# Optimization experiments

Hardware: AMD Instinct MI355X
Metric: run time of the kernel (lower is better)

The kernel has to match this reference:

```python
import jax, jax.numpy as jnp
import numpy as np

WS = (8, 8)          # window size
NHEAD = 6
D_MODEL = 192

def _rel_pos_index(ws):
    coords = np.stack(np.meshgrid(np.arange(ws[0]), np.arange(ws[1]), indexing='ij'))  # (2, wh, ww)
    cf = coords.reshape(2, -1)                          # (2, N)
    rel = cf[:, :, None] - cf[:, None, :]               # (2, N, N)
    rel = rel.transpose(1, 2, 0).astype(np.int64)       # (N, N, 2)
    rel[:, :, 0] += ws[0] - 1
    rel[:, :, 1] += ws[1] - 1
    rel[:, :, 0] *= 2 * ws[1] - 1
    return rel.sum(-1)                                  # (N, N)

REL_IDX = jnp.asarray(_rel_pos_index(WS))

def setup_inputs() -> dict:
    key = jax.random.key(0)
    ks = jax.random.split(key, 6)
    B, H, W, C = 4, 256, 256, D_MODEL
    x = jax.random.normal(ks[0], (B, H * W, C), dtype=jnp.float32)
    qkv_w = jax.random.normal(ks[1], (3 * C, C), dtype=jnp.float32) * 0.02
    qkv_b = jnp.zeros((3 * C,), dtype=jnp.float32)
    proj_w = jax.random.normal(ks[2], (C, C), dtype=jnp.float32) * 0.02
    proj_b = jnp.zeros((C,), dtype=jnp.float32)
    n_bias = (2 * WS[0] - 1) * (2 * WS[1] - 1)
    rpb_table = jax.random.normal(ks[3], (n_bias, NHEAD), dtype=jnp.float32) * 0.02
    return {"x": x, "qkv_w": qkv_w, "qkv_b": qkv_b, "proj_w": proj_w,
            "proj_b": proj_b, "rpb_table": rpb_table, "H": H, "W": W}

def reference(x, qkv_w, qkv_b, proj_w, proj_b, rpb_table, H, W):
    B, Ni, C = x.shape
    h, d = NHEAD, C // NHEAD
    wh, ww = WS
    nH, nW = H // wh, W // ww
    N = wh * ww
    # window partition: (B, H, W, C) -> (B*nH*nW, N, C)
    xw = x.reshape(B, nH, wh, nW, ww, C).transpose(0, 1, 3, 2, 4, 5).reshape(-1, N, C)
    qkv = xw @ qkv_w.T + qkv_b                           # (B_, N, 3C)
    B_ = xw.shape[0]
    qkv = qkv.reshape(B_, N, 3, h, d).transpose(2, 0, 3, 1, 4)  # (3, B_, h, N, d)
    q, k, v = qkv[0], qkv[1], qkv[2]
    scale = d ** -0.5
    attn = jnp.einsum('bhnd,bhmd->bhnm', q, k) * scale   # (B_, h, N, N)
    bias = rpb_table[REL_IDX.reshape(-1)].reshape(N, N, h).transpose(2, 0, 1)  # (h, N, N)
    attn = jax.nn.softmax(attn + bias[None], axis=-1)
    out = jnp.einsum('bhnm,bhmd->bhnd', attn, v)         # (B_, h, N, d)
    out = out.transpose(0, 2, 1, 3).reshape(B_, N, C)
    out = out @ proj_w.T + proj_b
    # window reverse: (B*nH*nW, N, C) -> (B, H*W, C)
    out = out.reshape(B, nH, nW, wh, ww, C).transpose(0, 1, 3, 2, 4, 5).reshape(B, Ni, C)
    return out
```

## Files before the change

### kernel.cpp

```cpp
#include <hip/hip_runtime.h>

#define CDIM 192
#define NHEAD 6

typedef __bf16 bf16x8 __attribute__((ext_vector_type(8)));
typedef float f32x4 __attribute__((ext_vector_type(4)));

#define HB     78848
#define Q_OFF  0
#define K_OFF  25600
#define VT_OFF 51200
#define SMEM_BYTES (2 * HB)
#define XS  200
#define QS  200
#define KS  200
#define VTS 72
#define AOS 200
#define PS  72
#define OFS 196
#define SCALE 0.17677669529663687f

__device__ __forceinline__ unsigned short f2b(float f) {
    unsigned int u = __float_as_uint(f);
    u = (u + 0x7FFFu + ((u >> 16) & 1u)) >> 16;
    return (unsigned short)u;
}

#define WS_W1   0
#define WS_W2   221184
#define WS_BIAS 294912

__global__ void prep(const float* __restrict__ qkv_w, const float* __restrict__ proj_w,
                     const float* __restrict__ rpb,
                     unsigned short* __restrict__ W1, unsigned short* __restrict__ W2,
                     float* __restrict__ BIAS) {
    int t = blockIdx.x * 256 + threadIdx.x;
    if (t < 110592) { W1[t] = f2b(qkv_w[t]); return; }
    t -= 110592;
    if (t < 36864)  { W2[t] = f2b(proj_w[t]); return; }
    t -= 36864;
    {
        int h = t >> 12, ij = t & 4095;
        int i = ij >> 6, j = ij & 63;
        int idx = ((i >> 3) - (j >> 3) + 7) * 15 + ((i & 7) - (j & 7) + 7);
        BIAS[t] = rpb[idx * NHEAD + h];
    }
}

__global__ __launch_bounds__(512)
void win_attn(const float* __restrict__ x,
              const unsigned short* __restrict__ qkv_w,
              const float* __restrict__ qkv_b,
              const unsigned short* __restrict__ proj_w,
              const float* __restrict__ proj_b,
              const float* __restrict__ bias,
              float* __restrict__ out)
{
    extern __shared__ __align__(16) char smem[];

    const int tid  = threadIdx.x;
    const int wv   = tid >> 6;
    const int lane = tid & 63;
    const int l15  = lane & 15;
    const int g    = lane >> 4;
    const int g4   = g << 2;
    const int g8   = g << 3;

    long long base[2];
    #pragma unroll
    for (int w = 0; w < 2; ++w) {
        int wid = blockIdx.x * 2 + w;
        int b   = wid >> 10;
        int wy  = (wid >> 5) & 31;
        int wx  = wid & 31;
        base[w] = (long long)(b * 65536 + wy * 8 * 256 + wx * 8) * CDIM;
    }

    #pragma unroll
    for (int w = 0; w < 2; ++w) {
        __bf16* xk = (__bf16*)(smem + w * HB + K_OFF);
        #pragma unroll
        for (int r = 0; r < 6; ++r) {
            int i = tid + r * 512;
            int t = i / 48, part = i - t * 48;
            int iy = t >> 3, ix = t & 7;
            f32x4 v = *(const f32x4*)(x + base[w] + (iy * 256 + ix) * CDIM + part * 4);
            __bf16* dst = xk + t * XS + part * 4;
            dst[0] = (__bf16)v[0]; dst[1] = (__bf16)v[1];
            dst[2] = (__bf16)v[2]; dst[3] = (__bf16)v[3];
        }
    }
    __syncthreads();

    {
        const int qstart_lut[8] = {0, 5, 10, 15, 20, 25, 30, 31};
        const int start = qstart_lut[wv];

        f32x4 acc[2][4][5];
        #pragma unroll
        for (int w = 0; w < 2; ++w)
            #pragma unroll
            for (int mt = 0; mt < 4; ++mt)
                #pragma unroll
                for (int jn = 0; jn < 5; ++jn)
                    acc[w][mt][jn] = (f32x4){0.f, 0.f, 0.f, 0.f};

        #pragma unroll
        for (int kk = 0; kk < 6; ++kk) {
            bf16x8 bw[5];
            #pragma unroll
            for (int jn = 0; jn < 5; ++jn) {
                int o = (start + jn) * 16 + l15;
                bw[jn] = *(const bf16x8*)((const __bf16*)qkv_w + o * CDIM + kk * 32 + g8);
            }
            #pragma unroll
            for (int w = 0; w < 2; ++w) {
                const __bf16* xk = (const __bf16*)(smem + w * HB + K_OFF);
                bf16x8 aa[4];
                #pragma unroll
                for (int mt = 0; mt < 4; ++mt)
                    aa[mt] = *(const bf16x8*)(xk + (mt * 16 + l15) * XS + kk * 32 + g8);
                #pragma unroll
                for (int jn = 0; jn < 5; ++jn)
                    #pragma unroll
                    for (int mt = 0; mt < 4; ++mt)
                        acc[w][mt][jn] = __builtin_amdgcn_mfma_f32_16x16x32_bf16(aa[mt], bw[jn], acc[w][mt][jn], 0, 0, 0);
            }
        }
        __syncthreads();

        #pragma unroll
        for (int jn = 0; jn < 5; ++jn) {
            int nt = start + jn;
            int o  = nt * 16 + l15;
            float qb = qkv_b[o];
            #pragma unroll
            for (int w = 0; w < 2; ++w) {
                __bf16* ql  = (__bf16*)(smem + w * HB + Q_OFF);
                __bf16* kl  = (__bf16*)(smem + w * HB + K_OFF);
                __bf16* vtw = (__bf16*)(smem + w * HB + VT_OFF);
                #pragma unroll
                for (int mt = 0; mt < 4; ++mt) {
                    #pragma unroll
                    for (int rr = 0; rr < 4; ++rr) {
                        int tr = mt * 16 + g4 + rr;
                        float val = acc[w][mt][jn][rr] + qb;
                        if (nt < 12)       ql[tr * QS + o] = (__bf16)val;
                        else if (nt < 24)  kl[tr * KS + (o - 192)] = (__bf16)val;
                        else               vtw[(o - 384) * VTS + tr] = (__bf16)val;
                    }
                }
            }
        }
    }
    __syncthreads();

    f32x4 sh[2][3][4];
    #pragma unroll
    for (int w = 0; w < 2; ++w) {
        const __bf16* ql = (const __bf16*)(smem + w * HB + Q_OFF);
        const __bf16* kl = (const __bf16*)(smem + w * HB + K_OFF);
        #pragma unroll
        for (int u = 0; u < 3; ++u) {
            int gu = wv * 3 + u;
            int hu = gu >> 2;
            int rb = gu & 3;

            bf16x8 aq = *(const bf16x8*)(ql + (rb * 16 + l15) * QS + hu * 32 + g8);
            #pragma unroll
            for (int ni = 0; ni < 4; ++ni) {
                bf16x8 bk = *(const bf16x8*)(kl + (ni * 16 + l15) * KS + hu * 32 + g8);
                sh[w][u][ni] = __builtin_amdgcn_mfma_f32_16x16x32_bf16(aq, bk, (f32x4){0.f, 0.f, 0.f, 0.f}, 0, 0, 0);
            }

            const float* brow = bias + hu * 4096;
            #pragma unroll
            for (int rr = 0; rr < 4; ++rr) {
                int row = rb * 16 + g4 + rr;
                float v0 = sh[w][u][0][rr] * SCALE + brow[row * 64 +  0 + l15];
                float v1 = sh[w][u][1][rr] * SCALE + brow[row * 64 + 16 + l15];
                float v2 = sh[w][u][2][rr] * SCALE + brow[row * 64 + 32 + l15];
                float v3 = sh[w][u][3][rr] * SCALE + brow[row * 64 + 48 + l15];
                float m = fmaxf(fmaxf(v0, v1), fmaxf(v2, v3));
                m = fmaxf(m, __shfl_xor(m, 1));
                m = fmaxf(m, __shfl_xor(m, 2));
                m = fmaxf(m, __shfl_xor(m, 4));
                m = fmaxf(m, __shfl_xor(m, 8));
                v0 = __expf(v0 - m); v1 = __expf(v1 - m);
                v2 = __expf(v2 - m); v3 = __expf(v3 - m);
                float s = v0 + v1 + v2 + v3;
                s += __shfl_xor(s, 1); s += __shfl_xor(s, 2);
                s += __shfl_xor(s, 4); s += __shfl_xor(s, 8);
                float inv = 1.0f / s;
                sh[w][u][0][rr] = v0 * inv;
                sh[w][u][1][rr] = v1 * inv;
                sh[w][u][2][rr] = v2 * inv;
                sh[w][u][3][rr] = v3 * inv;
            }
        }
    }
    __syncthreads();

    #pragma unroll
    for (int w = 0; w < 2; ++w) {
        __bf16* ph  = (__bf16*)(smem + w * HB + Q_OFF) + wv * (16 * PS);
        const __bf16* vtw = (const __bf16*)(smem + w * HB + VT_OFF);
        __bf16* aob = (__bf16*)(smem + w * HB + K_OFF);
        #pragma unroll
        for (int u = 0; u < 3; ++u) {
            int gu = wv * 3 + u;
            int hu = gu >> 2;
            int rb = gu & 3;

            #pragma unroll
            for (int rr = 0; rr < 4; ++rr) {
                int pr = (g4 + rr) * PS;
                ph[pr +  0 + l15] = (__bf16)sh[w][u][0][rr];
                ph[pr + 16 + l15] = (__bf16)sh[w][u][1][rr];
                ph[pr + 32 + l15] = (__bf16)sh[w][u][2][rr];
                ph[pr + 48 + l15] = (__bf16)sh[w][u][3][rr];
            }
            __threadfence_block();

            f32x4 oacc[2];
            oacc[0] = (f32x4){0.f, 0.f, 0.f, 0.f};
            oacc[1] = (f32x4){0.f, 0.f, 0.f, 0.f};
            #pragma unroll
            for (int kk = 0; kk < 2; ++kk) {
                bf16x8 pa = *(const bf16x8*)(ph + l15 * PS + kk * 32 + g8);
                #pragma unroll
                for (int nj = 0; nj < 2; ++nj) {
                    bf16x8 bv = *(const bf16x8*)(vtw + (hu * 32 + nj * 16 + l15) * VTS + kk * 32 + g8);
                    oacc[nj] = __builtin_amdgcn_mfma_f32_16x16x32_bf16(pa, bv, oacc[nj], 0, 0, 0);
                }
            }
            __threadfence_block();
            #pragma unroll
            for (int nj = 0; nj < 2; ++nj)
                #pragma unroll
                for (int rr = 0; rr < 4; ++rr)
                    aob[(rb * 16 + g4 + rr) * AOS + hu * 32 + nj * 16 + l15] = (__bf16)oacc[nj][rr];
        }
    }
    __syncthreads();

    {
        const int pstart_lut[8] = {0, 2, 4, 6, 8, 10, 10, 10};
        const int start = pstart_lut[wv];

        f32x4 pacc[2][4][2];
        #pragma unroll
        for (int w = 0; w < 2; ++w)
            #pragma unroll
            for (int mt = 0; mt < 4; ++mt)
                #pragma unroll
                for (int jn = 0; jn < 2; ++jn)
                    pacc[w][mt][jn] = (f32x4){0.f, 0.f, 0.f, 0.f};

        #pragma unroll
        for (int kk = 0; kk < 6; ++kk) {
            bf16x8 bw[2];
            #pragma unroll
            for (int jn = 0; jn < 2; ++jn) {
                int o = (start + jn) * 16 + l15;
                bw[jn] = *(const bf16x8*)((const __bf16*)proj_w + o * CDIM + kk * 32 + g8);
            }
            #pragma unroll
            for (int w = 0; w < 2; ++w) {
                const __bf16* aob = (const __bf16*)(smem + w * HB + K_OFF);
                bf16x8 aa[4];
                #pragma unroll
                for (int mt = 0; mt < 4; ++mt)
                    aa[mt] = *(const bf16x8*)(aob + (mt * 16 + l15) * AOS + kk * 32 + g8);
                #pragma unroll
                for (int jn = 0; jn < 2; ++jn)
                    #pragma unroll
                    for (int mt = 0; mt < 4; ++mt)
                        pacc[w][mt][jn] = __builtin_amdgcn_mfma_f32_16x16x32_bf16(aa[mt], bw[jn], pacc[w][mt][jn], 0, 0, 0);
            }
        }
        __syncthreads();

        #pragma unroll
        for (int jn = 0; jn < 2; ++jn) {
            int o = (start + jn) * 16 + l15;
            float pb = proj_b[o];
            #pragma unroll
            for (int w = 0; w < 2; ++w) {
                float* stagef = (float*)(smem + w * HB);
                #pragma unroll
                for (int mt = 0; mt < 4; ++mt)
                    #pragma unroll
                    for (int rr = 0; rr < 4; ++rr) {
                        int tr = mt * 16 + g4 + rr;
                        stagef[tr * OFS + o] = pacc[w][mt][jn][rr] + pb;
                    }
            }
        }
    }
    __syncthreads();

    #pragma unroll
    for (int w = 0; w < 2; ++w) {
        const float* stagef = (const float*)(smem + w * HB);
        #pragma unroll
        for (int r = 0; r < 6; ++r) {
            int i = tid + r * 512;
            int t = i / 48, part = i - t * 48;
            int iy = t >> 3, ix = t & 7;
            *(f32x4*)(out + base[w] + (iy * 256 + ix) * CDIM + part * 4) =
                *(const f32x4*)(stagef + t * OFS + part * 4);
        }
    }
}

extern "C" void kernel_launch(void* const* d_in, const int* in_sizes, int n_in,
                              void* d_out, int out_size, void* d_ws, size_t ws_size,
                              hipStream_t stream) {
    const float* x      = (const float*)d_in[0];
    const float* qkv_w  = (const float*)d_in[1];
    const float* qkv_b  = (const float*)d_in[2];
    const float* proj_w = (const float*)d_in[3];
    const float* proj_b = (const float*)d_in[4];
    const float* rpb    = (const float*)d_in[5];
    float* outp = (float*)d_out;

    char* ws = (char*)d_ws;
    unsigned short* W1 = (unsigned short*)(ws + WS_W1);
    unsigned short* W2 = (unsigned short*)(ws + WS_W2);
    float* BIAS = (float*)(ws + WS_BIAS);

    hipFuncSetAttribute((const void*)win_attn,
                        hipFuncAttributeMaxDynamicSharedMemorySize, SMEM_BYTES);

    prep<<<672, 256, 0, stream>>>(qkv_w, proj_w, rpb, W1, W2, BIAS);
    win_attn<<<2048, 512, SMEM_BYTES, stream>>>(x, W1, qkv_b, W2, proj_b, BIAS, outp);
}
```

Before: 371.7 us.

## Load x directly into MFMA operands and process windows sequentially to cut registers

The fp32 input tile is no longer staged through shared memory as bf16. Each wave now reads its x rows straight from global memory, converts them to bf16 in registers and feeds them to the QKV MFMAs, which removes the staging pass and one block barrier. The QKV and attention phases now run one window at a time, so the accumulator and score arrays are half as large, aiming to lower register pressure. The cost is that every wave re-reads the whole x tile from global memory or cache, and the weight fragments are loaded once per window instead of being shared across both.

```diff
diff --git a/kernel.cpp b/kernel.cpp
--- a/kernel.cpp
+++ b/kernel.cpp
@@ -11,7 +11,6 @@
 #define K_OFF  25600
 #define VT_OFF 51200
 #define SMEM_BYTES (2 * HB)
-#define XS  200
 #define QS  200
 #define KS  200
 #define VTS 72
@@ -24,6 +23,13 @@
     unsigned int u = __float_as_uint(f);
     u = (u + 0x7FFFu + ((u >> 16) & 1u)) >> 16;
     return (unsigned short)u;
+}
+
+__device__ __forceinline__ bf16x8 cvt8(f32x4 a, f32x4 b) {
+    bf16x8 r;
+    r[0] = (__bf16)a[0]; r[1] = (__bf16)a[1]; r[2] = (__bf16)a[2]; r[3] = (__bf16)a[3];
+    r[4] = (__bf16)b[0]; r[5] = (__bf16)b[1]; r[6] = (__bf16)b[2]; r[7] = (__bf16)b[3];
+    return r;
 }
 
 #define WS_W1   0
@@ -76,75 +82,58 @@
         base[w] = (long long)(b * 65536 + wy * 8 * 256 + wx * 8) * CDIM;
     }
 
-    #pragma unroll
-    for (int w = 0; w < 2; ++w) {
-        __bf16* xk = (__bf16*)(smem + w * HB + K_OFF);
-        #pragma unroll
-        for (int r = 0; r < 6; ++r) {
-            int i = tid + r * 512;
-            int t = i / 48, part = i - t * 48;
-            int iy = t >> 3, ix = t & 7;
-            f32x4 v = *(const f32x4*)(x + base[w] + (iy * 256 + ix) * CDIM + part * 4);
-            __bf16* dst = xk + t * XS + part * 4;
-            dst[0] = (__bf16)v[0]; dst[1] = (__bf16)v[1];
-            dst[2] = (__bf16)v[2]; dst[3] = (__bf16)v[3];
-        }
-    }
-    __syncthreads();
-
     {
         const int qstart_lut[8] = {0, 5, 10, 15, 20, 25, 30, 31};
         const int start = qstart_lut[wv];
 
-        f32x4 acc[2][4][5];
-        #pragma unroll
-        for (int w = 0; w < 2; ++w)
+        #pragma unroll
+        for (int w = 0; w < 2; ++w) {
+            const float* xr[4];
+            #pragma unroll
+            for (int mt = 0; mt < 4; ++mt) {
+                int t0 = mt * 16 + l15;
+                xr[mt] = x + base[w] + ((t0 >> 3) * 256 + (t0 & 7)) * CDIM;
+            }
+
+            f32x4 acc[4][5];
             #pragma unroll
             for (int mt = 0; mt < 4; ++mt)
                 #pragma unroll
                 for (int jn = 0; jn < 5; ++jn)
-                    acc[w][mt][jn] = (f32x4){0.f, 0.f, 0.f, 0.f};
-
-        #pragma unroll
-        for (int kk = 0; kk < 6; ++kk) {
-            bf16x8 bw[5];
-            #pragma unroll
-            for (int jn = 0; jn < 5; ++jn) {
-                int o = (start + jn) * 16 + l15;
-                bw[jn] = *(const bf16x8*)((const __bf16*)qkv_w + o * CDIM + kk * 32 + g8);
-            }
-            #pragma unroll
-            for (int w = 0; w < 2; ++w) {
-                const __bf16* xk = (const __bf16*)(smem + w * HB + K_OFF);
+                    acc[mt][jn] = (f32x4){0.f, 0.f, 0.f, 0.f};
+
+            #pragma unroll
+            for (int kk = 0; kk < 6; ++kk) {
                 bf16x8 aa[4];
                 #pragma unroll
-                for (int mt = 0; mt < 4; ++mt)
-                    aa[mt] = *(const bf16x8*)(xk + (mt * 16 + l15) * XS + kk * 32 + g8);
-                #pragma unroll
-                for (int jn = 0; jn < 5; ++jn)
+                for (int mt = 0; mt < 4; ++mt) {
+                    f32x4 lo = *(const f32x4*)(xr[mt] + kk * 32 + g8);
+                    f32x4 hi = *(const f32x4*)(xr[mt] + kk * 32 + g8 + 4);
+                    aa[mt] = cvt8(lo, hi);
+                }
+                #pragma unroll
+                for (int jn = 0; jn < 5; ++jn) {
+                    int o = (start + jn) * 16 + l15;
+                    bf16x8 bw = *(const bf16x8*)((const __bf16*)qkv_w + o * CDIM + kk * 32 + g8);
                     #pragma unroll
                     for (int mt = 0; mt < 4; ++mt)
-                        acc[w][mt][jn] = __builtin_amdgcn_mfma_f32_16x16x32_bf16(aa[mt], bw[jn], acc[w][mt][jn], 0, 0, 0);
-            }
-        }
-        __syncthreads();
-
-        #pragma unroll
-        for (int jn = 0; jn < 5; ++jn) {
-            int nt = start + jn;
-            int o  = nt * 16 + l15;
-            float qb = qkv_b[o];
-            #pragma unroll
-            for (int w = 0; w < 2; ++w) {
-                __bf16* ql  = (__bf16*)(smem + w * HB + Q_OFF);
-                __bf16* kl  = (__bf16*)(smem + w * HB + K_OFF);
-                __bf16* vtw = (__bf16*)(smem + w * HB + VT_OFF);
+                        acc[mt][jn] = __builtin_amdgcn_mfma_f32_16x16x32_bf16(aa[mt], bw, acc[mt][jn], 0, 0, 0);
+                }
+            }
+            __bf16* ql  = (__bf16*)(smem + w * HB + Q_OFF);
+            __bf16* kl  = (__bf16*)(smem + w * HB + K_OFF);
+            __bf16* vtw = (__bf16*)(smem + w * HB + VT_OFF);
+            #pragma unroll
+            for (int jn = 0; jn < 5; ++jn) {
+                int nt = start + jn;
+                int o  = nt * 16 + l15;
+                float qb = qkv_b[o];
                 #pragma unroll
                 for (int mt = 0; mt < 4; ++mt) {
                     #pragma unroll
                     for (int rr = 0; rr < 4; ++rr) {
                         int tr = mt * 16 + g4 + rr;
-                        float val = acc[w][mt][jn][rr] + qb;
+                        float val = acc[mt][jn][rr] + qb;
                         if (nt < 12)       ql[tr * QS + o] = (__bf16)val;
                         else if (nt < 24)  kl[tr * KS + (o - 192)] = (__bf16)val;
                         else               vtw[(o - 384) * VTS + tr] = (__bf16)val;
@@ -155,93 +144,94 @@
     }
     __syncthreads();
 
-    f32x4 sh[2][3][4];
-    #pragma unroll
-    for (int w = 0; w < 2; ++w) {
-        const __bf16* ql = (const __bf16*)(smem + w * HB + Q_OFF);
-        const __bf16* kl = (const __bf16*)(smem + w * HB + K_OFF);
-        #pragma unroll
-        for (int u = 0; u < 3; ++u) {
-            int gu = wv * 3 + u;
-            int hu = gu >> 2;
-            int rb = gu & 3;
-
-            bf16x8 aq = *(const bf16x8*)(ql + (rb * 16 + l15) * QS + hu * 32 + g8);
-            #pragma unroll
-            for (int ni = 0; ni < 4; ++ni) {
-                bf16x8 bk = *(const bf16x8*)(kl + (ni * 16 + l15) * KS + hu * 32 + g8);
-                sh[w][u][ni] = __builtin_amdgcn_mfma_f32_16x16x32_bf16(aq, bk, (f32x4){0.f, 0.f, 0.f, 0.f}, 0, 0, 0);
-            }
-
-            const float* brow = bias + hu * 4096;
-            #pragma unroll
-            for (int rr = 0; rr < 4; ++rr) {
-                int row = rb * 16 + g4 + rr;
-                float v0 = sh[w][u][0][rr] * SCALE + brow[row * 64 +  0 + l15];
-                float v1 = sh[w][u][1][rr] * SCALE + brow[row * 64 + 16 + l15];
-                float v2 = sh[w][u][2][rr] * SCALE + brow[row * 64 + 32 + l15];
-                float v3 = sh[w][u][3][rr] * SCALE + brow[row * 64 + 48 + l15];
-                float m = fmaxf(fmaxf(v0, v1), fmaxf(v2, v3));
-                m = fmaxf(m, __shfl_xor(m, 1));
-                m = fmaxf(m, __shfl_xor(m, 2));
-                m = fmaxf(m, __shfl_xor(m, 4));
-                m = fmaxf(m, __shfl_xor(m, 8));
-                v0 = __expf(v0 - m); v1 = __expf(v1 - m);
-                v2 = __expf(v2 - m); v3 = __expf(v3 - m);
-                float s = v0 + v1 + v2 + v3;
-                s += __shfl_xor(s, 1); s += __shfl_xor(s, 2);
-                s += __shfl_xor(s, 4); s += __shfl_xor(s, 8);
-                float inv = 1.0f / s;
-                sh[w][u][0][rr] = v0 * inv;
-                sh[w][u][1][rr] = v1 * inv;
-                sh[w][u][2][rr] = v2 * inv;
-                sh[w][u][3][rr] = v3 * inv;
-            }
-        }
-    }
-    __syncthreads();
-
-    #pragma unroll
-    for (int w = 0; w < 2; ++w) {
-        __bf16* ph  = (__bf16*)(smem + w * HB + Q_OFF) + wv * (16 * PS);
-        const __bf16* vtw = (const __bf16*)(smem + w * HB + VT_OFF);
-        __bf16* aob = (__bf16*)(smem + w * HB + K_OFF);
-        #pragma unroll
-        for (int u = 0; u < 3; ++u) {
-            int gu = wv * 3 + u;
-            int hu = gu >> 2;
-            int rb = gu & 3;
-
-            #pragma unroll
-            for (int rr = 0; rr < 4; ++rr) {
-                int pr = (g4 + rr) * PS;
-                ph[pr +  0 + l15] = (__bf16)sh[w][u][0][rr];
-                ph[pr + 16 + l15] = (__bf16)sh[w][u][1][rr];
-                ph[pr + 32 + l15] = (__bf16)sh[w][u][2][rr];
-                ph[pr + 48 + l15] = (__bf16)sh[w][u][3][rr];
-            }
-            __threadfence_block();
-
-            f32x4 oacc[2];
-            oacc[0] = (f32x4){0.f, 0.f, 0.f, 0.f};
-            oacc[1] = (f32x4){0.f, 0.f, 0.f, 0.f};
-            #pragma unroll
-            for (int kk = 0; kk < 2; ++kk) {
-                bf16x8 pa = *(const bf16x8*)(ph + l15 * PS + kk * 32 + g8);
-                #pragma unroll
-                for (int nj = 0; nj < 2; ++nj) {
-                    bf16x8 bv = *(const bf16x8*)(vtw + (hu * 32 + nj * 16 + l15) * VTS + kk * 32 + g8);
-                    oacc[nj] = __builtin_amdgcn_mfma_f32_16x16x32_bf16(pa, bv, oacc[nj], 0, 0, 0);
-                }
-            }
-            __threadfence_block();
-            #pragma unroll
-            for (int nj = 0; nj < 2; ++nj)
-                #pragma unroll
-                for (int rr = 0; rr < 4; ++rr)
-                    aob[(rb * 16 + g4 + rr) * AOS + hu * 32 + nj * 16 + l15] = (__bf16)oacc[nj][rr];
-        }
-    }
+    f32x4 sh[3][4];
+
+#define ATTN_A(w) { \
+        const __bf16* ql = (const __bf16*)(smem + (w) * HB + Q_OFF); \
+        const __bf16* kl = (const __bf16*)(smem + (w) * HB + K_OFF); \
+        _Pragma("unroll") \
+        for (int u = 0; u < 3; ++u) { \
+            int gu = wv * 3 + u; \
+            int hu = gu >> 2; \
+            int rb = gu & 3; \
+            bf16x8 aq = *(const bf16x8*)(ql + (rb * 16 + l15) * QS + hu * 32 + g8); \
+            _Pragma("unroll") \
+            for (int ni = 0; ni < 4; ++ni) { \
+                bf16x8 bk = *(const bf16x8*)(kl + (ni * 16 + l15) * KS + hu * 32 + g8); \
+                sh[u][ni] = __builtin_amdgcn_mfma_f32_16x16x32_bf16(aq, bk, (f32x4){0.f, 0.f, 0.f, 0.f}, 0, 0, 0); \
+            } \
+            const float* brow = bias + hu * 4096; \
+            _Pragma("unroll") \
+            for (int rr = 0; rr < 4; ++rr) { \
+                int row = rb * 16 + g4 + rr; \
+                float v0 = sh[u][0][rr] * SCALE + brow[row * 64 +  0 + l15]; \
+                float v1 = sh[u][1][rr] * SCALE + brow[row * 64 + 16 + l15]; \
+                float v2 = sh[u][2][rr] * SCALE + brow[row * 64 + 32 + l15]; \
+                float v3 = sh[u][3][rr] * SCALE + brow[row * 64 + 48 + l15]; \
+                float m = fmaxf(fmaxf(v0, v1), fmaxf(v2, v3)); \
+                m = fmaxf(m, __shfl_xor(m, 1)); \
+                m = fmaxf(m, __shfl_xor(m, 2)); \
+                m = fmaxf(m, __shfl_xor(m, 4)); \
+                m = fmaxf(m, __shfl_xor(m, 8)); \
+                v0 = __expf(v0 - m); v1 = __expf(v1 - m); \
+                v2 = __expf(v2 - m); v3 = __expf(v3 - m); \
+                float s = v0 + v1 + v2 + v3; \
+                s += __shfl_xor(s, 1); s += __shfl_xor(s, 2); \
+                s += __shfl_xor(s, 4); s += __shfl_xor(s, 8); \
+                float inv = 1.0f / s; \
+                sh[u][0][rr] = v0 * inv; \
+                sh[u][1][rr] = v1 * inv; \
+                sh[u][2][rr] = v2 * inv; \
+                sh[u][3][rr] = v3 * inv; \
+            } \
+        } \
+    }
+
+#define ATTN_B(w) { \
+        __bf16* ph  = (__bf16*)(smem + (w) * HB + Q_OFF) + wv * (16 * PS); \
+        const __bf16* vtw = (const __bf16*)(smem + (w) * HB + VT_OFF); \
+        __bf16* aob = (__bf16*)(smem + (w) * HB + K_OFF); \
+        _Pragma("unroll") \
+        for (int u = 0; u < 3; ++u) { \
+            int gu = wv * 3 + u; \
+            int hu = gu >> 2; \
+            int rb = gu & 3; \
+            _Pragma("unroll") \
+            for (int rr = 0; rr < 4; ++rr) { \
+                int pr = (g4 + rr) * PS; \
+                ph[pr +  0 + l15] = (__bf16)sh[u][0][rr]; \
+                ph[pr + 16 + l15] = (__bf16)sh[u][1][rr]; \
+                ph[pr + 32 + l15] = (__bf16)sh[u][2][rr]; \
+                ph[pr + 48 + l15] = (__bf16)sh[u][3][rr]; \
+            } \
+            __threadfence_block(); \
+            f32x4 oacc[2]; \
+            oacc[0] = (f32x4){0.f, 0.f, 0.f, 0.f}; \
+            oacc[1] = (f32x4){0.f, 0.f, 0.f, 0.f}; \
+            _Pragma("unroll") \
+            for (int kk = 0; kk < 2; ++kk) { \
+                bf16x8 pa = *(const bf16x8*)(ph + l15 * PS + kk * 32 + g8); \
+                _Pragma("unroll") \
+                for (int nj = 0; nj < 2; ++nj) { \
+                    bf16x8 bv = *(const bf16x8*)(vtw + (hu * 32 + nj * 16 + l15) * VTS + kk * 32 + g8); \
+                    oacc[nj] = __builtin_amdgcn_mfma_f32_16x16x32_bf16(pa, bv, oacc[nj], 0, 0, 0); \
+                } \
+            } \
+            __threadfence_block(); \
+            _Pragma("unroll") \
+            for (int nj = 0; nj < 2; ++nj) \
+                _Pragma("unroll") \
+                for (int rr = 0; rr < 4; ++rr) \
+                    aob[(rb * 16 + g4 + rr) * AOS + hu * 32 + nj * 16 + l15] = (__bf16)oacc[nj][rr]; \
+        } \
+    }
+
+    ATTN_A(0)
+    __syncthreads();
+    ATTN_B(0)
+    ATTN_A(1)
+    __syncthreads();
+    ATTN_B(1)
     __syncthreads();
 
     {
@@ -312,6 +302,8 @@
                 *(const f32x4*)(stagef + t * OFS + part * 4);
         }
     }
+#undef ATTN_A
+#undef ATTN_B
 }
 
 extern "C" void kernel_launch(void* const* d_in, const int* in_sizes, int n_in,
```

Measured after the change: 543.7 us. 46.3% more time.
